# Performance work log

Measured on AMD Instinct MI355X. Metric: run time of the kernel, lower is better.

The kernel has to match this reference:

```python
import jax, jax.numpy as jnp
import numpy as np

S_, H_, W_ = 7, 56, 56   # input_resolution
WS = 7                   # window_size
SHIFT = 3                # shift_size
GT = 1                   # gt_num (global tokens per window)
HEADS = 12
EPS = 1e-5


def _rel_pos_index(w):
    # replicates the torch buffer construction (incl. its 3*w-1 / 2*w-1 multipliers)
    coords = np.stack(np.meshgrid(np.arange(w), np.arange(w), np.arange(w), indexing='ij'))
    cf = coords.reshape(3, -1)
    rc = (cf[:, :, None] - cf[:, None, :]).transpose(1, 2, 0).astype(np.int64)
    rc += w - 1
    rc[..., 0] *= 3 * w - 1
    rc[..., 1] *= 2 * w - 1
    return rc.sum(-1)  # (w^3, w^3)


def _attn_mask(S, H, W, w, sh):
    # standard 3D shifted-window mask, built once from static shapes
    img = np.zeros((S, H, W))
    cnt = 0
    sls = (slice(0, -w), slice(-w, -sh), slice(-sh, None))
    for a in sls:
        for b in sls:
            for c in sls:
                img[a, b, c] = cnt
                cnt += 1
    m = img.reshape(S // w, w, H // w, w, W // w, w).transpose(0, 2, 4, 1, 3, 5).reshape(-1, w ** 3)
    d = m[:, None, :] - m[:, :, None]
    return np.where(d != 0, -100.0, 0.0).astype(np.float32)  # (nW, w^3, w^3)


def _ln(x, g, b):
    mu = jnp.mean(x, -1, keepdims=True)
    var = jnp.mean((x - mu) ** 2, -1, keepdims=True)
    return (x - mu) * jax.lax.rsqrt(var + EPS) * g + b


def setup_inputs() -> dict:
    key = jax.random.key(0)
    ks = jax.random.split(key, 7)
    C = 384
    hid = 4 * C
    L = S_ * H_ * W_
    nW = (S_ // WS) * (H_ // WS) * (W_ // WS)
    p = lambda k, shape: jax.random.normal(k, shape, jnp.float32) * 0.02
    return dict(
        x=jax.random.normal(ks[0], (1, L, C), jnp.float32),
        gt=jax.random.normal(ks[1], (nW, GT, C), jnp.float32),
        norm1_g=jnp.ones((C,), jnp.float32), norm1_b=jnp.zeros((C,), jnp.float32),
        qkv_w=p(ks[2], (C, 3 * C)), qkv_b=jnp.zeros((3 * C,), jnp.float32),
        bias_table=p(ks[3], ((2 * WS - 1) ** 3, HEADS)),
        proj_w=p(ks[4], (C, C)), proj_b=jnp.zeros((C,), jnp.float32),
        norm2_g=jnp.ones((C,), jnp.float32), norm2_b=jnp.zeros((C,), jnp.float32),
        fc1_w=p(ks[5], (C, hid)), fc1_b=jnp.zeros((hid,), jnp.float32),
        fc2_w=p(ks[6], (hid, C)), fc2_b=jnp.zeros((C,), jnp.float32),
    )


def _forward(x, gt, norm1_g, norm1_b, qkv_w, qkv_b, bias_table, proj_w, proj_b,
             norm2_g, norm2_b, fc1_w, fc1_b, fc2_w, fc2_b):
    B, L, C = x.shape
    h = HEADS
    d = C // h
    scale = d ** -0.5
    N_ = WS ** 3
    N = N_ + GT
    rpi = _rel_pos_index(WS)
    mask = jnp.asarray(_attn_mask(S_, H_, W_, WS, SHIFT))
    nW = mask.shape[0]

    shortcut = x
    xs = _ln(x, norm1_g, norm1_b).reshape(B, S_, H_, W_, C)
    xs = jnp.roll(xs, (-SHIFT, -SHIFT, -SHIFT), axis=(1, 2, 3))  # cyclic shift
    # window partition -> (B*nW, N_, C)
    xw = xs.reshape(B, S_ // WS, WS, H_ // WS, WS, W_ // WS, WS, C)
    xw = xw.transpose(0, 1, 3, 5, 2, 4, 6, 7).reshape(-1, N_, C)

    # --- WindowAttention with global tokens ---
    xc = jnp.concatenate([gt, xw], axis=1)  # (B*nW, N, C)
    qkv = (xc @ qkv_w + qkv_b).reshape(-1, N, 3, h, d).transpose(2, 0, 3, 1, 4)
    q, k, v = qkv[0] * scale, qkv[1], qkv[2]  # (B*nW, h, N, d)
    attn = jnp.einsum('bhnd,bhmd->bhnm', q, k)
    bias = bias_table[rpi.reshape(-1)].reshape(N_, N_, h).transpose(2, 0, 1)  # (h, N_, N_)
    bias = jnp.pad(bias, ((0, 0), (GT, 0), (GT, 0)))      # zeros on gt rows/cols == original submatrix add
    mpad = jnp.pad(mask, ((0, 0), (GT, 0), (GT, 0)))
    attn = attn + bias[None]
    attn = attn.reshape(B, nW, h, N, N) + mpad[None, :, None]
    attn = jax.nn.softmax(attn.reshape(-1, h, N, N), axis=-1)
    out = jnp.einsum('bhnm,bhmd->bhnd', attn, v).transpose(0, 2, 1, 3).reshape(-1, N, C)
    out = out @ proj_w + proj_b
    gt_out = out[:, :GT]
    xw = out[:, GT:]

    # window reverse + reverse shift
    xs = xw.reshape(B, S_ // WS, H_ // WS, W_ // WS, WS, WS, WS, C)
    xs = xs.transpose(0, 1, 4, 2, 5, 3, 6, 7).reshape(B, S_, H_, W_, C)
    xs = jnp.roll(xs, (SHIFT, SHIFT, SHIFT), axis=(1, 2, 3)).reshape(B, L, C)

    x = shortcut + xs  # drop_path = 0
    y = _ln(x, norm2_g, norm2_b)
    y = jax.nn.gelu(y @ fc1_w + fc1_b, approximate=False) @ fc2_w + fc2_b
    return x + y, gt_out


def reference(x, gt, norm1_g, norm1_b, qkv_w, qkv_b, bias_table, proj_w, proj_b,
              norm2_g, norm2_b, fc1_w, fc1_b, fc2_w, fc2_b):
    return _forward(x, gt, norm1_g, norm1_b, qkv_w, qkv_b, bias_table, proj_w, proj_b,
                    norm2_g, norm2_b, fc1_w, fc1_b, fc2_w, fc2_b)
```

## Files before the change

### kernel.cpp

```cpp
#include <hip/hip_runtime.h>
#include <math.h>

typedef __attribute__((ext_vector_type(8))) short short8;
typedef __attribute__((ext_vector_type(4))) float f32x4;

__device__ __forceinline__ float b2f(short s) {
    unsigned u = ((unsigned)(unsigned short)s) << 16;
    return __builtin_bit_cast(float, u);
}
__device__ __forceinline__ short f2b(float f) {
    unsigned u = __builtin_bit_cast(unsigned, f);
    u += 0x7FFFu + ((u >> 16) & 1u);
    return (short)(u >> 16);
}
__device__ __forceinline__ short f2bf(float f) {
    unsigned u = __builtin_bit_cast(unsigned, f);
    return (short)((u + 0x8000u) >> 16);
}
__device__ __forceinline__ void gload16(const void* g, void* l) {
    __builtin_amdgcn_global_load_lds(
        (const __attribute__((address_space(1))) unsigned int*)g,
        (__attribute__((address_space(3))) unsigned int*)l, 16, 0, 0);
}

__global__ __launch_bounds__(256) void transpose_w(const float* __restrict__ src,
                                                   short* __restrict__ dst,
                                                   int K, int N) {
    __shared__ short tile[32][33];
    const int kt = blockIdx.y * 32, nt = blockIdx.x * 32;
    const int tx = threadIdx.x & 31, ty = threadIdx.x >> 5;
    #pragma unroll
    for (int i = 0; i < 4; i++) {
        int k = kt + ty + 8 * i, n = nt + tx;
        short v = 0;
        if (k < K && n < N) v = f2b(src[(size_t)k * N + n]);
        tile[ty + 8 * i][tx] = v;
    }
    __syncthreads();
    #pragma unroll
    for (int i = 0; i < 4; i++) {
        int n = nt + ty + 8 * i, k = kt + tx;
        if (n < N && k < K) dst[(size_t)n * K + k] = tile[tx][ty + 8 * i];
    }
}

__global__ void bias_pre(const float* __restrict__ btab, float* __restrict__ btf) {
    int idx = blockIdx.x * 256 + threadIdx.x;
    if (idx >= 12 * 22 * 22 * 64) return;
    int lane = idx & 63, rem = idx >> 6;
    int nb = rem % 22; rem /= 22;
    int rt = rem % 22; int head = rem / 22;
    int j = nb * 16 + (lane & 15);
    int ibase = rt * 16 + (lane >> 4) * 4;
    f32x4 out;
    #pragma unroll
    for (int r = 0; r < 4; r++) {
        int i = ibase + r;
        float v;
        if (j >= 344) v = -1e30f;
        else if (i >= 344 || i == 0 || j == 0) v = 0.f;
        else {
            int ti = i - 1, tj = j - 1;
            int ai = ti / 49, bi = (ti % 49) / 7, ci = ti % 7;
            int aj = tj / 49, bj = (tj % 49) / 7, cj = tj % 7;
            int id3 = (ai - aj + 6) * 20 + (bi - bj + 6) * 13 + (ci - cj + 6);
            v = btab[id3 * 12 + head];
        }
        out[r] = v;
    }
    *(f32x4*)&btf[(size_t)idx * 4] = out;
}

__global__ void gid_pre(unsigned char* __restrict__ gid) {
    int idx = blockIdx.x * 256 + threadIdx.x;
    if (idx >= 64 * 352) return;
    int w = idx / 352, n = idx % 352;
    unsigned char g = 0;
    if (n >= 1 && n < 344) {
        int t = n - 1;
        int a = t / 49, bb = (t % 49) / 7, cc = t % 7;
        int hw = w >> 3, ww = w & 7;
        int h = hw * 7 + bb, wd = ww * 7 + cc;
        int gs = (a < 4) ? 1 : 2;
        int gh = (h < 49) ? 0 : ((h < 53) ? 1 : 2);
        int gw = (wd < 49) ? 0 : ((wd < 53) ? 1 : 2);
        g = (unsigned char)(gs * 9 + gh * 3 + gw);
    }
    gid[idx] = g;
}

__global__ __launch_bounds__(256) void ln1_window(
    const float* __restrict__ x, const float* __restrict__ gt,
    const float* __restrict__ g, const float* __restrict__ b,
    short* __restrict__ xc)
{
    int wid = threadIdx.x >> 6, lane = threadIdx.x & 63;
    int r = blockIdx.x * 4 + wid;
    int w = r / 344, n = r - w * 344;
    if (n == 0) {
        #pragma unroll
        for (int i = 0; i < 6; i++) {
            int c = lane + i * 64;
            xc[(size_t)r * 384 + c] = f2b(gt[(size_t)w * 384 + c]);
        }
        return;
    }
    int t = n - 1;
    int a = t / 49, rm = t - a * 49, bb = rm / 7, cc = rm - bb * 7;
    int hw = w >> 3, ww = w & 7;
    int s = (a < 4) ? a + 3 : a - 4;
    int h = hw * 7 + bb + 3; if (h >= 56) h -= 56;
    int wd = ww * 7 + cc + 3; if (wd >= 56) wd -= 56;
    const float* row = x + (size_t)((s * 56 + h) * 56 + wd) * 384;
    float v[6]; float sum = 0.f;
    #pragma unroll
    for (int i = 0; i < 6; i++) { v[i] = row[lane + i * 64]; sum += v[i]; }
    #pragma unroll
    for (int off = 32; off >= 1; off >>= 1) sum += __shfl_xor(sum, off);
    float mu = sum * (1.0f / 384.0f);
    float vs = 0.f;
    #pragma unroll
    for (int i = 0; i < 6; i++) { float d = v[i] - mu; vs += d * d; }
    #pragma unroll
    for (int off = 32; off >= 1; off >>= 1) vs += __shfl_xor(vs, off);
    float rstd = rsqrtf(vs * (1.0f / 384.0f) + 1e-5f);
    #pragma unroll
    for (int i = 0; i < 6; i++) {
        int c = lane + i * 64;
        float o = (v[i] - mu) * rstd * g[c] + b[c];
        xc[(size_t)r * 384 + c] = f2b(o);
    }
}

__global__ __launch_bounds__(256) void ln2_kernel(
    const float* __restrict__ xn, const float* __restrict__ g,
    const float* __restrict__ b, short* __restrict__ out)
{
    int wid = threadIdx.x >> 6, lane = threadIdx.x & 63;
    int r = blockIdx.x * 4 + wid;
    const float* row = xn + (size_t)r * 384;
    float v[6]; float sum = 0.f;
    #pragma unroll
    for (int i = 0; i < 6; i++) { v[i] = row[lane + i * 64]; sum += v[i]; }
    #pragma unroll
    for (int off = 32; off >= 1; off >>= 1) sum += __shfl_xor(sum, off);
    float mu = sum * (1.0f / 384.0f);
    float vs = 0.f;
    #pragma unroll
    for (int i = 0; i < 6; i++) { float d = v[i] - mu; vs += d * d; }
    #pragma unroll
    for (int off = 32; off >= 1; off >>= 1) vs += __shfl_xor(vs, off);
    float rstd = rsqrtf(vs * (1.0f / 384.0f) + 1e-5f);
    #pragma unroll
    for (int i = 0; i < 6; i++) {
        int c = lane + i * 64;
        float o = (v[i] - mu) * rstd * g[c] + b[c];
        out[(size_t)r * 384 + c] = f2b(o);
    }
}

template<int EPI, bool QS>
__global__ __launch_bounds__(256, 4) void gemm128(
    const short* __restrict__ A, const short* __restrict__ BT,
    const float* __restrict__ bias, void* __restrict__ Out,
    const void* __restrict__ P0, void* __restrict__ P1,
    int M, int N, int K)
{
    __shared__ short As[128 * 64];
    __shared__ short Bs[128 * 64];
    const int m0 = blockIdx.y * 128, n0 = blockIdx.x * 128;
    const int tid = threadIdx.x;
    const int wid = tid >> 6, lane = tid & 63;
    const int wm = wid >> 1, wn = wid & 1;
    const int l15 = lane & 15, quad = lane >> 4;

    f32x4 acc[4][4];
    #pragma unroll
    for (int i = 0; i < 4; i++)
        #pragma unroll
        for (int j = 0; j < 4; j++) acc[i][j] = (f32x4){0.f, 0.f, 0.f, 0.f};

    const int trow = tid >> 3;
    const int cs = tid & 7;
    const int gc = cs ^ (trow & 7);
    const short* Ag[4]; const short* Bg[4];
    #pragma unroll
    for (int j = 0; j < 4; j++) {
        int ar = m0 + j * 32 + trow; if (ar >= M) ar = M - 1;
        Ag[j] = A + (size_t)ar * K + gc * 8;
        Bg[j] = BT + (size_t)(n0 + j * 32 + trow) * K + gc * 8;
    }
    short* AsW[4]; short* BsW[4];
    #pragma unroll
    for (int j = 0; j < 4; j++) {
        AsW[j] = &As[(j * 32 + wid * 8) * 64];
        BsW[j] = &Bs[(j * 32 + wid * 8) * 64];
    }
    int arow[4], brow[4];
    #pragma unroll
    for (int mt = 0; mt < 4; mt++) arow[mt] = wm * 64 + mt * 16 + l15;
    #pragma unroll
    for (int nt = 0; nt < 4; nt++) brow[nt] = wn * 64 + nt * 16 + l15;

    for (int ks = 0; ks < K; ks += 64) {
        #pragma unroll
        for (int j = 0; j < 4; j++) gload16(Ag[j] + ks, AsW[j]);
        #pragma unroll
        for (int j = 0; j < 4; j++) gload16(Bg[j] + ks, BsW[j]);
        __syncthreads();
        #pragma unroll
        for (int ko = 0; ko < 2; ko++) {
            short8 af[4], bf[4];
            #pragma unroll
            for (int mt = 0; mt < 4; mt++)
                af[mt] = *(const short8*)&As[arow[mt] * 64
                         + (((ko * 4 + quad) ^ (l15 & 7)) * 8)];
            #pragma unroll
            for (int nt = 0; nt < 4; nt++)
                bf[nt] = *(const short8*)&Bs[brow[nt] * 64
                         + (((ko * 4 + quad) ^ (l15 & 7)) * 8)];
            #pragma unroll
            for (int mt = 0; mt < 4; mt++)
                #pragma unroll
                for (int nt = 0; nt < 4; nt++)
                    acc[mt][nt] = __builtin_amdgcn_mfma_f32_16x16x32_bf16(
                        af[mt], bf[nt], acc[mt][nt], 0, 0, 0);
        }
        __syncthreads();
    }

    #pragma unroll
    for (int mt = 0; mt < 4; mt++) {
        #pragma unroll
        for (int nt = 0; nt < 4; nt++) {
            #pragma unroll
            for (int r = 0; r < 4; r++) {
                int row = m0 + wm * 64 + mt * 16 + quad * 4 + r;
                int col = n0 + wn * 64 + nt * 16 + l15;
                if (row >= M) continue;
                float v = acc[mt][nt][r] + bias[col];
                if (EPI == 0) {
                    if (QS && col < 384) v *= 0.17677669529663687f;
                    ((short*)Out)[(size_t)row * N + col] = f2b(v);
                } else if (EPI == 1) {
                    float u2 = v * v;
                    float w  = v * fmaf(0.07135481633f, u2, 1.5957691216f);
                    float e  = __expf(w);
                    float t  = __builtin_amdgcn_rcpf(1.0f + e);
                    v = v - v * t;
                    ((short*)Out)[(size_t)row * N + col] = f2b(v);
                } else if (EPI == 2) {
                    int w = row / 344, n = row - w * 344;
                    if (n == 0) {
                        ((float*)P1)[(size_t)w * 384 + col] = v;
                    } else {
                        int t = n - 1;
                        int a = t / 49, rm = t - a * 49;
                        int bb = rm / 7, cc = rm - bb * 7;
                        int hw = w >> 3, ww = w & 7;
                        int s = (a < 4) ? a + 3 : a - 4;
                        int h = hw * 7 + bb + 3; if (h >= 56) h -= 56;
                        int wd = ww * 7 + cc + 3; if (wd >= 56) wd -= 56;
                        size_t td = (size_t)((s * 56 + h) * 56 + wd) * 384 + col;
                        ((float*)Out)[td] = v + ((const float*)P0)[td];
                    }
                } else {
                    v += ((const float*)P0)[(size_t)row * N + col];
                    ((float*)Out)[(size_t)row * N + col] = v;
                }
            }
        }
    }
}

__global__ __launch_bounds__(256) void attn_kernel(
    const short* __restrict__ qkv, const float* __restrict__ btf,
    const unsigned char* __restrict__ gid, short* __restrict__ attn_out)
{
    __shared__ short KT[352 * 32];
    __shared__ short VT[32 * 360];
    __shared__ short Pbuf[4 * 2 * 16 * 32];
    __shared__ unsigned char Gs[352];
    const int blk = blockIdx.x;
    const int w = blk / 12, head = blk - w * 12;
    const int tid = threadIdx.x;
    const int wid = tid >> 6, lane = tid & 63;
    const int l15 = lane & 15, quad = lane >> 4;
    const size_t base = (size_t)w * 344 * 1152 + head * 32;

    for (int c = tid; c < 352 * 4; c += 256) {
        int row = c >> 2, ch = c & 3;
        short8 v8 = (short8){0,0,0,0,0,0,0,0};
        if (row < 344) v8 = *(const short8*)&qkv[base + 384 + (size_t)row * 1152 + ch * 8];
        int slot = ch ^ ((row >> 1) & 3);
        *(short8*)&KT[row * 32 + slot * 8] = v8;
    }
    for (int e = tid; e < 344 * 4; e += 256) {
        int key = e >> 2, g = (e & 3) * 8;
        short8 v8 = *(const short8*)&qkv[base + 768 + (size_t)key * 1152 + g];
        #pragma unroll
        for (int i = 0; i < 8; i++) VT[(g + i) * 360 + key] = v8[i];
    }
    for (int e = tid; e < 8 * 32; e += 256) {
        int key = 344 + (e >> 5), dd = e & 31;
        VT[dd * 360 + key] = 0;
    }
    for (int e = tid; e < 352; e += 256) Gs[e] = gid[w * 352 + e];
    __syncthreads();

    const float* bh = btf + (size_t)head * (22 * 22 * 256);
    short* PwA = &Pbuf[wid * 1024];
    short* PwB = PwA + 512;

    const int cl = l15 & 7, c0 = l15 >> 3, c1 = c0 | 2;
    const int sw0 = (quad * 2) & 3, sw1 = sw0 | 1;
    const int swq = (l15 >> 1) & 3;
    const int paOff = l15 * 32 + ((quad ^ swq) * 8);
    const int ktOff = l15 * 32 + ((quad ^ swq) * 8);
    const int o0r01 = ((c0 ^ sw0) * 8) + cl, o0r23 = ((c0 ^ sw1) * 8) + cl;
    const int o1r01 = ((c1 ^ sw0) * 8) + cl, o1r23 = ((c1 ^ sw1) * 8) + cl;

    for (int j = wid; j < 11; j += 4) {
        const int rtA = 2 * j, rtB = rtA + 1;
        const int qrA = rtA * 16 + l15;
        int qrB = rtB * 16 + l15; if (qrB > 343) qrB = 343;
        short8 afA = *(const short8*)&qkv[base + (size_t)qrA * 1152 + quad * 8];
        short8 afB = *(const short8*)&qkv[base + (size_t)qrB * 1152 + quad * 8];

        int rgA[4], rgB[4]; bool ipA[4];
        #pragma unroll
        for (int r = 0; r < 4; r++) {
            int iA = rtA * 16 + quad * 4 + r;
            rgA[r] = Gs[iA]; ipA[r] = (iA > 0);
            rgB[r] = Gs[iA + 16];
        }

        f32x4 oA0 = {0,0,0,0}, oA1 = {0,0,0,0}, oB0 = {0,0,0,0}, oB1 = {0,0,0,0};
        float lA[4] = {0,0,0,0}, lB[4] = {0,0,0,0};
        const float* bhA = bh + (size_t)rtA * (22 * 256);
        const float* bhB = bh + (size_t)rtB * (22 * 256);

        for (int kk = 0; kk < 11; kk++) {
            const int nb0 = kk * 2, nb1 = nb0 + 1;
            f32x4 bA0 = *(const f32x4*)&bhA[(size_t)(nb0 * 64 + lane) * 4];
            f32x4 bA1 = *(const f32x4*)&bhA[(size_t)(nb1 * 64 + lane) * 4];
            f32x4 bB0 = *(const f32x4*)&bhB[(size_t)(nb0 * 64 + lane) * 4];
            f32x4 bB1 = *(const f32x4*)&bhB[(size_t)(nb1 * 64 + lane) * 4];
            short8 k0 = *(const short8*)&KT[nb0 * 512 + ktOff];
            short8 k1 = *(const short8*)&KT[nb1 * 512 + ktOff];
            f32x4 sA0 = __builtin_amdgcn_mfma_f32_16x16x32_bf16(afA, k0, bA0, 0, 0, 0);
            f32x4 sA1 = __builtin_amdgcn_mfma_f32_16x16x32_bf16(afA, k1, bA1, 0, 0, 0);
            f32x4 sB0 = __builtin_amdgcn_mfma_f32_16x16x32_bf16(afB, k0, bB0, 0, 0, 0);
            f32x4 sB1 = __builtin_amdgcn_mfma_f32_16x16x32_bf16(afB, k1, bB1, 0, 0, 0);

            int j0 = kk * 32 + l15;
            int cg0 = Gs[j0], cg1 = Gs[j0 + 16];
            bool jp0 = (j0 > 0);
            #pragma unroll
            for (int r = 0; r < 4; r++) {
                float pA0 = __expf(sA0[r]); if (jp0 && ipA[r] && rgA[r] != cg0) pA0 = 0.f;
                float pA1 = __expf(sA1[r]); if (ipA[r] && rgA[r] != cg1) pA1 = 0.f;
                float pB0 = __expf(sB0[r]); if (jp0 && rgB[r] != cg0) pB0 = 0.f;
                float pB1 = __expf(sB1[r]); if (rgB[r] != cg1) pB1 = 0.f;
                lA[r] += pA0 + pA1;
                lB[r] += pB0 + pB1;
                int rowb = (quad * 4 + r) * 32;
                int oo0 = (r < 2) ? o0r01 : o0r23;
                int oo1 = (r < 2) ? o1r01 : o1r23;
                PwA[rowb + oo0] = f2bf(pA0);
                PwA[rowb + oo1] = f2bf(pA1);
                PwB[rowb + oo0] = f2bf(pB0);
                PwB[rowb + oo1] = f2bf(pB1);
            }
            short8 paA = *(const short8*)&PwA[paOff];
            short8 paB = *(const short8*)&PwB[paOff];
            short8 v0 = *(const short8*)&VT[l15 * 360 + kk * 32 + quad * 8];
            short8 v1 = *(const short8*)&VT[(16 + l15) * 360 + kk * 32 + quad * 8];
            oA0 = __builtin_amdgcn_mfma_f32_16x16x32_bf16(paA, v0, oA0, 0, 0, 0);
            oA1 = __builtin_amdgcn_mfma_f32_16x16x32_bf16(paA, v1, oA1, 0, 0, 0);
            oB0 = __builtin_amdgcn_mfma_f32_16x16x32_bf16(paB, v0, oB0, 0, 0, 0);
            oB1 = __builtin_amdgcn_mfma_f32_16x16x32_bf16(paB, v1, oB1, 0, 0, 0);
        }

        #pragma unroll
        for (int r = 0; r < 4; r++) {
            lA[r] += __shfl_xor(lA[r], 1); lA[r] += __shfl_xor(lA[r], 2);
            lA[r] += __shfl_xor(lA[r], 4); lA[r] += __shfl_xor(lA[r], 8);
            lB[r] += __shfl_xor(lB[r], 1); lB[r] += __shfl_xor(lB[r], 2);
            lB[r] += __shfl_xor(lB[r], 4); lB[r] += __shfl_xor(lB[r], 8);
        }
        #pragma unroll
        for (int r = 0; r < 4; r++) {
            int rowA = rtA * 16 + quad * 4 + r;
            float invA = 1.0f / lA[r];
            size_t obA = ((size_t)w * 344 + rowA) * 384 + head * 32;
            attn_out[obA + l15] = f2b(oA0[r] * invA);
            attn_out[obA + 16 + l15] = f2b(oA1[r] * invA);
            int rowB = rowA + 16;
            if (rowB < 344) {
                float invB = 1.0f / lB[r];
                size_t obB = ((size_t)w * 344 + rowB) * 384 + head * 32;
                attn_out[obB + l15] = f2b(oB0[r] * invB);
                attn_out[obB + 16 + l15] = f2b(oB1[r] * invB);
            }
        }
    }
}

extern "C" void kernel_launch(void* const* d_in, const int* in_sizes, int n_in,
                              void* d_out, int out_size, void* d_ws, size_t ws_size,
                              hipStream_t stream)
{
    const float* x      = (const float*)d_in[0];
    const float* gt     = (const float*)d_in[1];
    const float* n1g    = (const float*)d_in[2];
    const float* n1b    = (const float*)d_in[3];
    const float* qkv_w  = (const float*)d_in[4];
    const float* qkv_b  = (const float*)d_in[5];
    const float* btab   = (const float*)d_in[6];
    const float* proj_w = (const float*)d_in[7];
    const float* proj_b = (const float*)d_in[8];
    const float* n2g    = (const float*)d_in[9];
    const float* n2b    = (const float*)d_in[10];
    const float* fc1_w  = (const float*)d_in[11];
    const float* fc1_b  = (const float*)d_in[12];
    const float* fc2_w  = (const float*)d_in[13];
    const float* fc2_b  = (const float*)d_in[14];

    char* ws = (char*)d_ws;
    short* wt_qkv  = (short*)(ws + 0);
    short* wt_proj = (short*)(ws + 884736);
    short* wt_fc1  = (short*)(ws + 1179648);
    short* wt_fc2  = (short*)(ws + 2359296);
    short* xc      = (short*)(ws + 3538944);
    short* qkvb    = (short*)(ws + 20447232);
    short* attn_o  = xc;
    short* h1      = (short*)(ws + 3538944);
    float* xnew    = (float*)(ws + 71172096);
    float* btf     = (float*)(ws + 71172096);
    unsigned char* gidb = (unsigned char*)(ws + 77119488);
    short* xnorm   = (short*)(ws + 104890368);

    float* outx  = (float*)d_out;
    float* outgt = outx + (size_t)21952 * 384;

    transpose_w<<<dim3(36, 12), 256, 0, stream>>>(qkv_w, wt_qkv, 384, 1152);
    transpose_w<<<dim3(12, 12), 256, 0, stream>>>(proj_w, wt_proj, 384, 384);
    transpose_w<<<dim3(48, 12), 256, 0, stream>>>(fc1_w, wt_fc1, 384, 1536);
    transpose_w<<<dim3(12, 48), 256, 0, stream>>>(fc2_w, wt_fc2, 1536, 384);

    bias_pre<<<dim3((12 * 22 * 22 * 64 + 255) / 256), 256, 0, stream>>>(btab, btf);
    gid_pre<<<dim3((64 * 352 + 255) / 256), 256, 0, stream>>>(gidb);

    ln1_window<<<dim3(5504), 256, 0, stream>>>(x, gt, n1g, n1b, xc);

    gemm128<0, true><<<dim3(9, 172), 256, 0, stream>>>(xc, wt_qkv, qkv_b, qkvb,
                                                       nullptr, nullptr, 22016, 1152, 384);

    attn_kernel<<<dim3(768), 256, 0, stream>>>(qkvb, btf, gidb, attn_o);

    gemm128<2, false><<<dim3(3, 172), 256, 0, stream>>>(attn_o, wt_proj, proj_b, xnew,
                                                        x, outgt, 22016, 384, 384);

    ln2_kernel<<<dim3(5488), 256, 0, stream>>>(xnew, n2g, n2b, xnorm);

    gemm128<1, false><<<dim3(12, 172), 256, 0, stream>>>(xnorm, wt_fc1, fc1_b, h1,
                                                         nullptr, nullptr, 21952, 1536, 384);

    gemm128<3, false><<<dim3(3, 172), 256, 0, stream>>>(h1, wt_fc2, fc2_b, outx,
                                                        xnew, nullptr, 21952, 384, 1536);
}
```

Before: 428.1 us.

## Fold shift mask into bias table and keep softmax probs in registers

Precomputes a combined bias-plus-mask table for each of the four window classes (interior, edge-H, edge-W, corner), so the attention kernel no longer needs the group-id buffer or per-element mask compares. It swaps the QK MFMA operand order and permutes the K rows in LDS so the score fragment layout matches the A-operand layout of the PV MFMA. Probabilities are then packed to bf16 with v_cvt_pk_bf16_f32 directly in registers instead of going through an LDS round-trip. The bias table grows fourfold and the mask is now subtracted as -100 instead of zeroing probabilities, which changes the numerics slightly but matches the reference.

```diff
diff --git a/kernel.cpp b/kernel.cpp
--- a/kernel.cpp
+++ b/kernel.cpp
@@ -3,6 +3,7 @@
 
 typedef __attribute__((ext_vector_type(8))) short short8;
 typedef __attribute__((ext_vector_type(4))) float f32x4;
+typedef __attribute__((ext_vector_type(4))) int i32x4;
 
 __device__ __forceinline__ float b2f(short s) {
     unsigned u = ((unsigned)(unsigned short)s) << 16;
@@ -13,9 +14,10 @@
     u += 0x7FFFu + ((u >> 16) & 1u);
     return (short)(u >> 16);
 }
-__device__ __forceinline__ short f2bf(float f) {
-    unsigned u = __builtin_bit_cast(unsigned, f);
-    return (short)((u + 0x8000u) >> 16);
+__device__ __forceinline__ int cvtpk(float lo, float hi) {
+    int d;
+    asm("v_cvt_pk_bf16_f32 %0, %1, %2" : "=v"(d) : "v"(lo), "v"(hi));
+    return d;
 }
 __device__ __forceinline__ void gload16(const void* g, void* l) {
     __builtin_amdgcn_global_load_lds(
@@ -46,47 +48,37 @@
 
 __global__ void bias_pre(const float* __restrict__ btab, float* __restrict__ btf) {
     int idx = blockIdx.x * 256 + threadIdx.x;
-    if (idx >= 12 * 22 * 22 * 64) return;
-    int lane = idx & 63, rem = idx >> 6;
-    int nb = rem % 22; rem /= 22;
-    int rt = rem % 22; int head = rem / 22;
-    int j = nb * 16 + (lane & 15);
-    int ibase = rt * 16 + (lane >> 4) * 4;
+    if (idx >= 4 * 12 * 22 * 11 * 2 * 64) return;
+    int lane = idx & 63; int rem = idx >> 6;
+    int h = rem & 1; rem >>= 1;
+    int kk = rem % 11; rem /= 11;
+    int rt = rem % 22; rem /= 22;
+    int head = rem % 12; int cls = rem / 12;
+    int i = rt * 16 + (lane & 15);
+    int jbase = kk * 32 + (lane >> 4) * 8 + h * 4;
     f32x4 out;
     #pragma unroll
     for (int r = 0; r < 4; r++) {
-        int i = ibase + r;
+        int jj = jbase + r;
         float v;
-        if (j >= 344) v = -1e30f;
-        else if (i >= 344 || i == 0 || j == 0) v = 0.f;
+        if (jj >= 344) v = -1e30f;
+        else if (i >= 344 || i == 0 || jj == 0) v = 0.f;
         else {
-            int ti = i - 1, tj = j - 1;
+            int ti = i - 1, tj = jj - 1;
             int ai = ti / 49, bi = (ti % 49) / 7, ci = ti % 7;
             int aj = tj / 49, bj = (tj % 49) / 7, cj = tj % 7;
             int id3 = (ai - aj + 6) * 20 + (bi - bj + 6) * 13 + (ci - cj + 6);
             v = btab[id3 * 12 + head];
+            int gsi = (ai < 4) ? 1 : 2, gsj = (aj < 4) ? 1 : 2;
+            int ghi = (cls & 2) ? ((bi < 4) ? 1 : 2) : 0;
+            int ghj = (cls & 2) ? ((bj < 4) ? 1 : 2) : 0;
+            int gwi = (cls & 1) ? ((ci < 4) ? 1 : 2) : 0;
+            int gwj = (cls & 1) ? ((cj < 4) ? 1 : 2) : 0;
+            if (gsi != gsj || ghi != ghj || gwi != gwj) v -= 100.f;
         }
         out[r] = v;
     }
     *(f32x4*)&btf[(size_t)idx * 4] = out;
-}
-
-__global__ void gid_pre(unsigned char* __restrict__ gid) {
-    int idx = blockIdx.x * 256 + threadIdx.x;
-    if (idx >= 64 * 352) return;
-    int w = idx / 352, n = idx % 352;
-    unsigned char g = 0;
-    if (n >= 1 && n < 344) {
-        int t = n - 1;
-        int a = t / 49, bb = (t % 49) / 7, cc = t % 7;
-        int hw = w >> 3, ww = w & 7;
-        int h = hw * 7 + bb, wd = ww * 7 + cc;
-        int gs = (a < 4) ? 1 : 2;
-        int gh = (h < 49) ? 0 : ((h < 53) ? 1 : 2);
-        int gw = (wd < 49) ? 0 : ((wd < 53) ? 1 : 2);
-        g = (unsigned char)(gs * 9 + gh * 3 + gw);
-    }
-    gid[idx] = g;
 }
 
 __global__ __launch_bounds__(256) void ln1_window(
@@ -274,26 +266,26 @@
 }
 
 __global__ __launch_bounds__(256) void attn_kernel(
-    const short* __restrict__ qkv, const float* __restrict__ btf,
-    const unsigned char* __restrict__ gid, short* __restrict__ attn_out)
+    const short* __restrict__ qkv, const float* __restrict__ btfm,
+    short* __restrict__ attn_out)
 {
     __shared__ short KT[352 * 32];
     __shared__ short VT[32 * 360];
-    __shared__ short Pbuf[4 * 2 * 16 * 32];
-    __shared__ unsigned char Gs[352];
     const int blk = blockIdx.x;
     const int w = blk / 12, head = blk - w * 12;
+    const int cls = (((w >> 3) == 7) ? 2 : 0) | (((w & 7) == 7) ? 1 : 0);
     const int tid = threadIdx.x;
     const int wid = tid >> 6, lane = tid & 63;
     const int l15 = lane & 15, quad = lane >> 4;
     const size_t base = (size_t)w * 344 * 1152 + head * 32;
 
     for (int c = tid; c < 352 * 4; c += 256) {
-        int row = c >> 2, ch = c & 3;
+        int n = c >> 2, ch = c & 3;
         short8 v8 = (short8){0,0,0,0,0,0,0,0};
-        if (row < 344) v8 = *(const short8*)&qkv[base + 384 + (size_t)row * 1152 + ch * 8];
-        int slot = ch ^ ((row >> 1) & 3);
-        *(short8*)&KT[row * 32 + slot * 8] = v8;
+        if (n < 344) v8 = *(const short8*)&qkv[base + 384 + (size_t)n * 1152 + ch * 8];
+        int j32 = n & 31, kk = n >> 5;
+        int R = kk * 32 + ((j32 >> 2) & 1) * 16 + ((j32 >> 3) << 2) + (j32 & 3);
+        *(short8*)&KT[R * 32 + ((ch ^ ((R >> 1) & 3)) * 8)] = v8;
     }
     for (int e = tid; e < 344 * 4; e += 256) {
         int key = e >> 2, g = (e & 3) * 8;
@@ -305,20 +297,11 @@
         int key = 344 + (e >> 5), dd = e & 31;
         VT[dd * 360 + key] = 0;
     }
-    for (int e = tid; e < 352; e += 256) Gs[e] = gid[w * 352 + e];
     __syncthreads();
 
-    const float* bh = btf + (size_t)head * (22 * 22 * 256);
-    short* PwA = &Pbuf[wid * 1024];
-    short* PwB = PwA + 512;
-
-    const int cl = l15 & 7, c0 = l15 >> 3, c1 = c0 | 2;
-    const int sw0 = (quad * 2) & 3, sw1 = sw0 | 1;
+    const float* bh = btfm + (size_t)(cls * 12 + head) * (22 * 11 * 2 * 256);
     const int swq = (l15 >> 1) & 3;
-    const int paOff = l15 * 32 + ((quad ^ swq) * 8);
-    const int ktOff = l15 * 32 + ((quad ^ swq) * 8);
-    const int o0r01 = ((c0 ^ sw0) * 8) + cl, o0r23 = ((c0 ^ sw1) * 8) + cl;
-    const int o1r01 = ((c1 ^ sw0) * 8) + cl, o1r23 = ((c1 ^ sw1) * 8) + cl;
+    const int kOff = l15 * 32 + ((quad ^ swq) * 8);
 
     for (int j = wid; j < 11; j += 4) {
         const int rtA = 2 * j, rtB = rtA + 1;
@@ -327,53 +310,43 @@
         short8 afA = *(const short8*)&qkv[base + (size_t)qrA * 1152 + quad * 8];
         short8 afB = *(const short8*)&qkv[base + (size_t)qrB * 1152 + quad * 8];
 
-        int rgA[4], rgB[4]; bool ipA[4];
-        #pragma unroll
-        for (int r = 0; r < 4; r++) {
-            int iA = rtA * 16 + quad * 4 + r;
-            rgA[r] = Gs[iA]; ipA[r] = (iA > 0);
-            rgB[r] = Gs[iA + 16];
-        }
-
         f32x4 oA0 = {0,0,0,0}, oA1 = {0,0,0,0}, oB0 = {0,0,0,0}, oB1 = {0,0,0,0};
-        float lA[4] = {0,0,0,0}, lB[4] = {0,0,0,0};
-        const float* bhA = bh + (size_t)rtA * (22 * 256);
-        const float* bhB = bh + (size_t)rtB * (22 * 256);
+        float lA = 0.f, lB = 0.f;
+        const float* bhA = bh + (size_t)rtA * (11 * 2 * 256) + lane * 4;
+        const float* bhB = bh + (size_t)rtB * (11 * 2 * 256) + lane * 4;
 
         for (int kk = 0; kk < 11; kk++) {
-            const int nb0 = kk * 2, nb1 = nb0 + 1;
-            f32x4 bA0 = *(const f32x4*)&bhA[(size_t)(nb0 * 64 + lane) * 4];
-            f32x4 bA1 = *(const f32x4*)&bhA[(size_t)(nb1 * 64 + lane) * 4];
-            f32x4 bB0 = *(const f32x4*)&bhB[(size_t)(nb0 * 64 + lane) * 4];
-            f32x4 bB1 = *(const f32x4*)&bhB[(size_t)(nb1 * 64 + lane) * 4];
-            short8 k0 = *(const short8*)&KT[nb0 * 512 + ktOff];
-            short8 k1 = *(const short8*)&KT[nb1 * 512 + ktOff];
-            f32x4 sA0 = __builtin_amdgcn_mfma_f32_16x16x32_bf16(afA, k0, bA0, 0, 0, 0);
-            f32x4 sA1 = __builtin_amdgcn_mfma_f32_16x16x32_bf16(afA, k1, bA1, 0, 0, 0);
-            f32x4 sB0 = __builtin_amdgcn_mfma_f32_16x16x32_bf16(afB, k0, bB0, 0, 0, 0);
-            f32x4 sB1 = __builtin_amdgcn_mfma_f32_16x16x32_bf16(afB, k1, bB1, 0, 0, 0);
-
-            int j0 = kk * 32 + l15;
-            int cg0 = Gs[j0], cg1 = Gs[j0 + 16];
-            bool jp0 = (j0 > 0);
-            #pragma unroll
-            for (int r = 0; r < 4; r++) {
-                float pA0 = __expf(sA0[r]); if (jp0 && ipA[r] && rgA[r] != cg0) pA0 = 0.f;
-                float pA1 = __expf(sA1[r]); if (ipA[r] && rgA[r] != cg1) pA1 = 0.f;
-                float pB0 = __expf(sB0[r]); if (jp0 && rgB[r] != cg0) pB0 = 0.f;
-                float pB1 = __expf(sB1[r]); if (rgB[r] != cg1) pB1 = 0.f;
-                lA[r] += pA0 + pA1;
-                lB[r] += pB0 + pB1;
-                int rowb = (quad * 4 + r) * 32;
-                int oo0 = (r < 2) ? o0r01 : o0r23;
-                int oo1 = (r < 2) ? o1r01 : o1r23;
-                PwA[rowb + oo0] = f2bf(pA0);
-                PwA[rowb + oo1] = f2bf(pA1);
-                PwB[rowb + oo0] = f2bf(pB0);
-                PwB[rowb + oo1] = f2bf(pB1);
-            }
-            short8 paA = *(const short8*)&PwA[paOff];
-            short8 paB = *(const short8*)&PwB[paOff];
+            f32x4 cA0 = *(const f32x4*)&bhA[(kk * 2 + 0) * 256];
+            f32x4 cA1 = *(const f32x4*)&bhA[(kk * 2 + 1) * 256];
+            f32x4 cB0 = *(const f32x4*)&bhB[(kk * 2 + 0) * 256];
+            f32x4 cB1 = *(const f32x4*)&bhB[(kk * 2 + 1) * 256];
+            short8 k0 = *(const short8*)&KT[kk * 1024 + kOff];
+            short8 k1 = *(const short8*)&KT[kk * 1024 + 512 + kOff];
+            f32x4 sA0 = __builtin_amdgcn_mfma_f32_16x16x32_bf16(k0, afA, cA0, 0, 0, 0);
+            f32x4 sA1 = __builtin_amdgcn_mfma_f32_16x16x32_bf16(k1, afA, cA1, 0, 0, 0);
+            f32x4 sB0 = __builtin_amdgcn_mfma_f32_16x16x32_bf16(k0, afB, cB0, 0, 0, 0);
+            f32x4 sB1 = __builtin_amdgcn_mfma_f32_16x16x32_bf16(k1, afB, cB1, 0, 0, 0);
+
+            float a0 = __expf(sA0[0]), a1 = __expf(sA0[1]);
+            float a2 = __expf(sA0[2]), a3 = __expf(sA0[3]);
+            float a4 = __expf(sA1[0]), a5 = __expf(sA1[1]);
+            float a6 = __expf(sA1[2]), a7 = __expf(sA1[3]);
+            lA += ((a0 + a1) + (a2 + a3)) + ((a4 + a5) + (a6 + a7));
+            i32x4 pkA;
+            pkA[0] = cvtpk(a0, a1); pkA[1] = cvtpk(a2, a3);
+            pkA[2] = cvtpk(a4, a5); pkA[3] = cvtpk(a6, a7);
+            short8 paA = __builtin_bit_cast(short8, pkA);
+
+            float b0 = __expf(sB0[0]), b1 = __expf(sB0[1]);
+            float b2 = __expf(sB0[2]), b3 = __expf(sB0[3]);
+            float b4 = __expf(sB1[0]), b5 = __expf(sB1[1]);
+            float b6 = __expf(sB1[2]), b7 = __expf(sB1[3]);
+            lB += ((b0 + b1) + (b2 + b3)) + ((b4 + b5) + (b6 + b7));
+            i32x4 pkB;
+            pkB[0] = cvtpk(b0, b1); pkB[1] = cvtpk(b2, b3);
+            pkB[2] = cvtpk(b4, b5); pkB[3] = cvtpk(b6, b7);
+            short8 paB = __builtin_bit_cast(short8, pkB);
+
             short8 v0 = *(const short8*)&VT[l15 * 360 + kk * 32 + quad * 8];
             short8 v1 = *(const short8*)&VT[(16 + l15) * 360 + kk * 32 + quad * 8];
             oA0 = __builtin_amdgcn_mfma_f32_16x16x32_bf16(paA, v0, oA0, 0, 0, 0);
@@ -382,26 +355,22 @@
             oB1 = __builtin_amdgcn_mfma_f32_16x16x32_bf16(paB, v1, oB1, 0, 0, 0);
         }
 
-        #pragma unroll
-        for (int r = 0; r < 4; r++) {
-            lA[r] += __shfl_xor(lA[r], 1); lA[r] += __shfl_xor(lA[r], 2);
-            lA[r] += __shfl_xor(lA[r], 4); lA[r] += __shfl_xor(lA[r], 8);
-            lB[r] += __shfl_xor(lB[r], 1); lB[r] += __shfl_xor(lB[r], 2);
-            lB[r] += __shfl_xor(lB[r], 4); lB[r] += __shfl_xor(lB[r], 8);
-        }
+        lA += __shfl_xor(lA, 16); lA += __shfl_xor(lA, 32);
+        lB += __shfl_xor(lB, 16); lB += __shfl_xor(lB, 32);
+        float iA = 1.0f / lA, iB = 1.0f / lB;
         #pragma unroll
         for (int r = 0; r < 4; r++) {
             int rowA = rtA * 16 + quad * 4 + r;
-            float invA = 1.0f / lA[r];
+            float nA = __shfl(iA, quad * 4 + r);
+            float nB = __shfl(iB, quad * 4 + r);
             size_t obA = ((size_t)w * 344 + rowA) * 384 + head * 32;
-            attn_out[obA + l15] = f2b(oA0[r] * invA);
-            attn_out[obA + 16 + l15] = f2b(oA1[r] * invA);
+            attn_out[obA + l15] = f2b(oA0[r] * nA);
+            attn_out[obA + 16 + l15] = f2b(oA1[r] * nA);
             int rowB = rowA + 16;
             if (rowB < 344) {
-                float invB = 1.0f / lB[r];
                 size_t obB = ((size_t)w * 344 + rowB) * 384 + head * 32;
-                attn_out[obB + l15] = f2b(oB0[r] * invB);
-                attn_out[obB + 16 + l15] = f2b(oB1[r] * invB);
+                attn_out[obB + l15] = f2b(oB0[r] * nB);
+                attn_out[obB + 16 + l15] = f2b(oB1[r] * nB);
             }
         }
     }
@@ -437,8 +406,7 @@
     short* attn_o  = xc;
     short* h1      = (short*)(ws + 3538944);
     float* xnew    = (float*)(ws + 71172096);
-    float* btf     = (float*)(ws + 71172096);
-    unsigned char* gidb = (unsigned char*)(ws + 77119488);
+    float* btfm    = (float*)(ws + 71172096);
     short* xnorm   = (short*)(ws + 104890368);
 
     float* outx  = (float*)d_out;
@@ -449,15 +417,14 @@
     transpose_w<<<dim3(48, 12), 256, 0, stream>>>(fc1_w, wt_fc1, 384, 1536);
     transpose_w<<<dim3(12, 48), 256, 0, stream>>>(fc2_w, wt_fc2, 1536, 384);
 
-    bias_pre<<<dim3((12 * 22 * 22 * 64 + 255) / 256), 256, 0, stream>>>(btab, btf);
-    gid_pre<<<dim3((64 * 352 + 255) / 256), 256, 0, stream>>>(gidb);
+    bias_pre<<<dim3((4 * 12 * 22 * 11 * 2 * 64 + 255) / 256), 256, 0, stream>>>(btab, btfm);
 
     ln1_window<<<dim3(5504), 256, 0, stream>>>(x, gt, n1g, n1b, xc);
 
     gemm128<0, true><<<dim3(9, 172), 256, 0, stream>>>(xc, wt_qkv, qkv_b, qkvb,
                                                        nullptr, nullptr, 22016, 1152, 384);
 
-    attn_kernel<<<dim3(768), 256, 0, stream>>>(qkvb, btf, gidb, attn_o);
+    attn_kernel<<<dim3(768), 256, 0, stream>>>(qkvb, btfm, attn_o);
 
     gemm128<2, false><<<dim3(3, 172), 256, 0, stream>>>(attn_o, wt_proj, proj_b, xnew,
                                                         x, outgt, 22016, 384, 384);
```

Measured after the change: 415.9 us. 1.03x faster.
